# Kernel optimization log

Measured on AMD Instinct MI355X. Metric: run time of the kernel, lower is better.

## Reference

```python
import jax, jax.numpy as jnp
import numpy as np

B, T, H = 8, 8192, 512
E, R = 4, 16
SCALE = 0.04  # ~1/sqrt(H), keeps activations/logits in a sane range


def setup_inputs() -> dict:
    key = jax.random.key(0)
    ks = jax.random.split(key, 7)
    return {
        "x": jax.random.normal(ks[0], (B, T, H), jnp.float32),
        "gate_w": jax.random.normal(ks[1], (E, H), jnp.float32) * SCALE,
        "thr_w": jax.random.normal(ks[2], (1, H), jnp.float32) * SCALE,
        "fc1_w": jax.random.normal(ks[3], (E, H, H), jnp.float32) * SCALE,
        "lora_A": jax.random.normal(ks[4], (E, H, R), jnp.float32) * SCALE,
        "lora_B": jax.random.normal(ks[5], (E, R, H), jnp.float32) * SCALE,
        "fc2_w": jax.random.normal(ks[6], (E, H, H), jnp.float32) * SCALE,
    }


def reference(x, gate_w, thr_w, fc1_w, lora_A, lora_B, fc2_w):
    b, t, h = x.shape
    e = gate_w.shape[0]
    xf = x.reshape(-1, h)  # [N, H], N = B*T

    # Threshold-gated routing
    gate_logits = jax.nn.softmax(xf @ gate_w.T, axis=-1)          # [N, E]
    thresholds = jax.nn.sigmoid(xf @ thr_w.T) * (1.0 / e)         # [N, 1]
    adapted = gate_logits - thresholds                            # [N, E]
    selected = (adapted >= 0).astype(xf.dtype)                    # [N, E]
    weights = adapted * selected
    wsum = jnp.sum(weights, axis=-1, keepdims=True)
    wsum = jnp.where(wsum == 0, jnp.ones_like(wsum), wsum)
    weights = weights / wsum                                      # [N, E]

    # Experts: fc2(relu(fc1(x)) @ A @ B). Dense over all experts; the
    # weighted combine with zero weights matches the gather/scatter path.
    hidden = jax.nn.relu(jnp.einsum('ni,ehi->neh', xf, fc1_w))    # [N, E, H]
    lo = jnp.einsum('neh,ehr->ner', hidden, lora_A)               # [N, E, R]
    lo = jnp.einsum('ner,ero->neo', lo, lora_B)                   # [N, E, H]
    expert_out = jnp.einsum('neo,edo->ned', lo, fc2_w)            # [N, E, H]

    out = jnp.einsum('ne,ned->nd', weights, expert_out)           # [N, H]
    return out.reshape(b, t, h)
```

## Files before the change

kernel.cpp:

```cpp
#include <hip/hip_runtime.h>
#include <stdint.h>

#define NTOK 65536
#define HD   512
#define EXP  4
#define RK   16

typedef __attribute__((ext_vector_type(8)))  short short8;
typedef __attribute__((ext_vector_type(4)))  float f32x4;
typedef __attribute__((ext_vector_type(16))) float f32x16;

__device__ __forceinline__ unsigned short f2bf(float f) {
  union { float f; unsigned int u; } c; c.f = f;
  return (unsigned short)((c.u + 0x7fffu + ((c.u >> 16) & 1u)) >> 16);
}

__device__ __forceinline__ void gl_lds16(const void* g, void* l) {
  __builtin_amdgcn_global_load_lds((const __attribute__((address_space(1))) void*)g,
                                   (__attribute__((address_space(3))) void*)l, 16, 0, 0);
}

__global__ void convgate(const float* __restrict__ x, const float* __restrict__ gw,
                         const float* __restrict__ tw, unsigned short* __restrict__ xbo,
                         float* __restrict__ gates) {
  const int lane = threadIdx.x & 63;
  const int n = blockIdx.x * 4 + (threadIdx.x >> 6);
  const float4* xr = (const float4*)(x + (size_t)n * HD);
  const float4 xa = xr[lane * 2], xb = xr[lane * 2 + 1];
  ushort4 ua, ub;
  ua.x = f2bf(xa.x); ua.y = f2bf(xa.y); ua.z = f2bf(xa.z); ua.w = f2bf(xa.w);
  ub.x = f2bf(xb.x); ub.y = f2bf(xb.y); ub.z = f2bf(xb.z); ub.w = f2bf(xb.w);
  ushort4* xo = (ushort4*)(xbo + (size_t)n * HD);
  xo[lane * 2] = ua; xo[lane * 2 + 1] = ub;
  float s[5];
#pragma unroll
  for (int e = 0; e < 4; e++) {
    const float4* wr = (const float4*)(gw + e * HD);
    const float4 wa = wr[lane * 2], wb = wr[lane * 2 + 1];
    s[e] = xa.x * wa.x + xa.y * wa.y + xa.z * wa.z + xa.w * wa.w
         + xb.x * wb.x + xb.y * wb.y + xb.z * wb.z + xb.w * wb.w;
  }
  {
    const float4* wr = (const float4*)tw;
    const float4 wa = wr[lane * 2], wb = wr[lane * 2 + 1];
    s[4] = xa.x * wa.x + xa.y * wa.y + xa.z * wa.z + xa.w * wa.w
         + xb.x * wb.x + xb.y * wb.y + xb.z * wb.z + xb.w * wb.w;
  }
#pragma unroll
  for (int off = 32; off > 0; off >>= 1)
#pragma unroll
    for (int i = 0; i < 5; i++) s[i] += __shfl_xor(s[i], off, 64);
  float m = fmaxf(fmaxf(s[0], s[1]), fmaxf(s[2], s[3]));
  float e0 = expf(s[0] - m), e1 = expf(s[1] - m), e2 = expf(s[2] - m), e3 = expf(s[3] - m);
  float inv = 1.f / (e0 + e1 + e2 + e3);
  float thr = 0.25f / (1.f + expf(-s[4]));
  float a0 = e0 * inv - thr, a1 = e1 * inv - thr, a2 = e2 * inv - thr, a3 = e3 * inv - thr;
  float w0 = a0 > 0.f ? a0 : 0.f, w1 = a1 > 0.f ? a1 : 0.f;
  float w2 = a2 > 0.f ? a2 : 0.f, w3 = a3 > 0.f ? a3 : 0.f;
  float wsum = w0 + w1 + w2 + w3;
  wsum = (wsum == 0.f) ? 1.f : wsum;
  if (lane < 4) {
    float wv = lane == 0 ? w0 : lane == 1 ? w1 : lane == 2 ? w2 : w3;
    gates[(size_t)n * 4 + lane] = wv / wsum;
  }
}

__global__ void convk(const float* __restrict__ in, unsigned short* __restrict__ o, int n4) {
  int i = blockIdx.x * 256 + threadIdx.x;
  if (i < n4) {
    float4 v = ((const float4*)in)[i];
    ushort4 u;
    u.x = f2bf(v.x); u.y = f2bf(v.y); u.z = f2bf(v.z); u.w = f2bf(v.w);
    ((ushort4*)o)[i] = u;
  }
}

__global__ void prep_mt(const float* __restrict__ loraB, const float* __restrict__ fc2,
                        unsigned short* __restrict__ Mt) {
  int idx = blockIdx.x * 256 + threadIdx.x;
  int d  = idx & (HD - 1);
  int er = idx >> 9;
  int e = er >> 4, r = er & 15;
  const float4* B = (const float4*)(loraB + ((size_t)e * RK + r) * HD);
  const float4* F = (const float4*)(fc2 + ((size_t)e * HD + d) * HD);
  float a0 = 0.f, a1 = 0.f, a2 = 0.f, a3 = 0.f;
  for (int i = 0; i < HD / 4; i += 4) {
    float4 b0 = B[i],     f0 = F[i];
    float4 b1 = B[i + 1], f1 = F[i + 1];
    float4 b2 = B[i + 2], f2 = F[i + 2];
    float4 b3 = B[i + 3], f3 = F[i + 3];
    a0 += b0.x * f0.x + b0.y * f0.y + b0.z * f0.z + b0.w * f0.w;
    a1 += b1.x * f1.x + b1.y * f1.y + b1.z * f1.z + b1.w * f1.w;
    a2 += b2.x * f2.x + b2.y * f2.y + b2.z * f2.z + b2.w * f2.w;
    a3 += b3.x * f3.x + b3.y * f3.y + b3.z * f3.z + b3.w * f3.w;
  }
  Mt[d * 64 + er] = f2bf(a0 + a1 + a2 + a3);
}

__launch_bounds__(256, 4)
__global__ void fc1_lora(const unsigned short* __restrict__ xb,
                         const unsigned short* __restrict__ w1b,
                         const float* __restrict__ loraA,
                         float* __restrict__ lw) {
  __shared__ __align__(16) char smem[34816];
  const int bid = blockIdx.x;
  const int c = bid & 7, s = bid >> 3;
  const int eh = s & 15;
  const int e = eh >> 2, hq = eh & 3;
  const int ntile = ((s >> 4) << 3) | c;
  const int n0 = ntile * 128;
  const int tid = threadIdx.x;
  const int wave = tid >> 6, lane = tid & 63;
  const int l16 = lane & 15, quad = lane >> 4;
  const int l32 = lane & 31, half = lane >> 5;

  const unsigned short* xg = xb + (size_t)n0 * HD;
  const unsigned short* wg = w1b + ((size_t)e * HD + (size_t)hq * 128) * HD;

  char* ldsx = smem;
  char* ldsw = smem + 16384;

  const unsigned short* xsrc[4];
  const unsigned short* wsrc[4];
#pragma unroll
  for (int i = 0; i < 4; i++) {
    const int sl = tid + 256 * i;
    const int row = sl >> 3, g = (sl & 7) ^ (row & 7);
    xsrc[i] = xg + (size_t)row * HD + g * 8;
    wsrc[i] = wg + (size_t)row * HD + g * 8;
  }

  const int twave = (wave & 1) * 64;
  const int hwave = (wave >> 1) * 64;

  int axo[4][2], bxo[4][2];
#pragma unroll
  for (int kk = 0; kk < 4; kk++)
#pragma unroll
    for (int b = 0; b < 2; b++) {
      const int rowa = twave + b * 32 + l32;
      axo[kk][b] = (rowa * 8 + ((kk * 2 + half) ^ (rowa & 7))) * 16;
      const int rowb = hwave + b * 32 + l32;
      bxo[kk][b] = (rowb * 8 + ((kk * 2 + half) ^ (rowb & 7))) * 16;
    }

  f32x16 acc[2][2];
#pragma unroll
  for (int mb = 0; mb < 2; mb++)
#pragma unroll
    for (int nb = 0; nb < 2; nb++)
#pragma unroll
      for (int r = 0; r < 16; r++) acc[mb][nb][r] = 0.f;

  for (int ks = 0; ks < 8; ks++) {
    const int ko = ks * 64;
#pragma unroll
    for (int i = 0; i < 4; i++) {
      gl_lds16(xsrc[i] + ko, ldsx + (256 * i + wave * 64) * 16);
      gl_lds16(wsrc[i] + ko, ldsw + (256 * i + wave * 64) * 16);
    }
    __syncthreads();
#pragma unroll
    for (int kk = 0; kk < 4; kk++) {
      short8 af[2], bf[2];
#pragma unroll
      for (int mb = 0; mb < 2; mb++) af[mb] = *(const short8*)(ldsx + axo[kk][mb]);
#pragma unroll
      for (int nb = 0; nb < 2; nb++) bf[nb] = *(const short8*)(ldsw + bxo[kk][nb]);
#pragma unroll
      for (int mb = 0; mb < 2; mb++)
#pragma unroll
        for (int nb = 0; nb < 2; nb++)
          acc[mb][nb] = __builtin_amdgcn_mfma_f32_32x32x16_bf16(af[mb], bf[nb], acc[mb][nb], 0, 0, 0);
    }
    __syncthreads();
  }

  unsigned short* hsm = (unsigned short*)smem;
#pragma unroll
  for (int mb = 0; mb < 2; mb++)
#pragma unroll
    for (int nb = 0; nb < 2; nb++) {
      const int colh = hwave + nb * 32 + l32;
#pragma unroll
      for (int r = 0; r < 16; r++) {
        const int tok = twave + mb * 32 + 4 * half + (r & 3) + 8 * (r >> 2);
        float v = acc[mb][nb][r];
        v = v > 0.f ? v : 0.f;
        hsm[tok * 136 + colh] = f2bf(v);
      }
    }
  __syncthreads();

  const float* Ae = loraA + (size_t)e * HD * RK;
  const int hA0 = hq * 128;
  f32x4 lo[2];
#pragma unroll
  for (int mf = 0; mf < 2; mf++)
#pragma unroll
    for (int i = 0; i < 4; i++) lo[mf][i] = 0.f;
#pragma unroll
  for (int k2 = 0; k2 < 4; k2++) {
    short8 a2[2];
#pragma unroll
    for (int mf = 0; mf < 2; mf++) {
      const int tok = wave * 32 + mf * 16 + l16;
      a2[mf] = *(const short8*)(hsm + tok * 136 + k2 * 32 + quad * 8);
    }
    union { short8 v; unsigned short s[8]; } b2;
#pragma unroll
    for (int j = 0; j < 8; j++)
      b2.s[j] = f2bf(Ae[(size_t)(hA0 + k2 * 32 + quad * 8 + j) * RK + l16]);
#pragma unroll
    for (int mf = 0; mf < 2; mf++)
      lo[mf] = __builtin_amdgcn_mfma_f32_16x16x32_bf16(a2[mf], b2.v, lo[mf], 0, 0, 0);
  }
#pragma unroll
  for (int mf = 0; mf < 2; mf++)
#pragma unroll
    for (int i = 0; i < 4; i++)
      atomicAdd(lw + (size_t)(n0 + wave * 32 + mf * 16 + quad * 4 + i) * 64 + e * 16 + l16, lo[mf][i]);
}

__launch_bounds__(256, 2)
__global__ void combine_k(const float* __restrict__ lw, const float* __restrict__ gates,
                          const unsigned short* __restrict__ Mt, float* __restrict__ out) {
  __shared__ __align__(16) char smem[65536];
  const int n0 = blockIdx.x * 64;
  const int tid = threadIdx.x;
  const int wave = tid >> 6, lane = tid & 63, quad = lane >> 4, l16 = lane & 15;
#pragma unroll
  for (int i = 0; i < 16; i++) {
    const int slot = tid + 256 * i;
    const int row = slot >> 3;
    const int g = (slot & 7) ^ (row & 7);
    *(uint4*)(smem + slot * 16) = *(const uint4*)(Mt + row * 64 + g * 8);
  }
  __syncthreads();
  f32x4 acc[4][8];
#pragma unroll
  for (int a = 0; a < 4; a++)
#pragma unroll
    for (int b = 0; b < 8; b++)
#pragma unroll
      for (int i = 0; i < 4; i++) acc[a][b][i] = 0.f;
#pragma unroll
  for (int ks = 0; ks < 2; ks++) {
    short8 af[4], bfr[8];
#pragma unroll
    for (int mf = 0; mf < 4; mf++) {
      const int n = n0 + mf * 16 + l16;
      const float* lr = lw + (size_t)n * 64 + ks * 32 + quad * 8;
      float4 u0 = *(const float4*)lr;
      float4 u1 = *(const float4*)(lr + 4);
      const float g = gates[(size_t)n * 4 + ((ks * 32 + quad * 8) >> 4)];
      union { short8 v; unsigned short s[8]; } a;
      a.s[0] = f2bf(u0.x * g); a.s[1] = f2bf(u0.y * g);
      a.s[2] = f2bf(u0.z * g); a.s[3] = f2bf(u0.w * g);
      a.s[4] = f2bf(u1.x * g); a.s[5] = f2bf(u1.y * g);
      a.s[6] = f2bf(u1.z * g); a.s[7] = f2bf(u1.w * g);
      af[mf] = a.v;
    }
#pragma unroll
    for (int nf = 0; nf < 8; nf++) {
      const int row = wave * 128 + nf * 16 + l16;
      const int slot = row * 8 + ((ks * 4 + quad) ^ (row & 7));
      bfr[nf] = *(const short8*)(smem + slot * 16);
    }
#pragma unroll
    for (int mf = 0; mf < 4; mf++)
#pragma unroll
      for (int nf = 0; nf < 8; nf++)
        acc[mf][nf] = __builtin_amdgcn_mfma_f32_16x16x32_bf16(af[mf], bfr[nf], acc[mf][nf], 0, 0, 0);
  }
#pragma unroll
  for (int mf = 0; mf < 4; mf++)
#pragma unroll
    for (int nf = 0; nf < 8; nf++) {
      const int d = wave * 128 + nf * 16 + l16;
#pragma unroll
      for (int i = 0; i < 4; i++)
        out[(size_t)(n0 + mf * 16 + quad * 4 + i) * HD + d] = acc[mf][nf][i];
    }
}

extern "C" void kernel_launch(void* const* d_in, const int* in_sizes, int n_in,
                              void* d_out, int out_size, void* d_ws, size_t ws_size,
                              hipStream_t stream) {
  const float* x      = (const float*)d_in[0];
  const float* gate_w = (const float*)d_in[1];
  const float* thr_w  = (const float*)d_in[2];
  const float* fc1_w  = (const float*)d_in[3];
  const float* lora_A = (const float*)d_in[4];
  const float* lora_B = (const float*)d_in[5];
  const float* fc2_w  = (const float*)d_in[6];
  float* out = (float*)d_out;
  char* ws = (char*)d_ws;

  unsigned short* xbp = (unsigned short*)(ws);
  unsigned short* w1b = (unsigned short*)(ws + 67108864);
  unsigned short* Mt  = (unsigned short*)(ws + 69206016);
  float*          gts = (float*)(ws + 69271552);
  float*          lwp = (float*)(ws + 70320128);

  hipMemsetAsync(lwp, 0, (size_t)NTOK * 64 * sizeof(float), stream);
  convgate<<<NTOK / 4, 256, 0, stream>>>(x, gate_w, thr_w, xbp, gts);
  convk<<<1024, 256, 0, stream>>>(fc1_w, w1b, EXP * HD * HD / 4);
  prep_mt<<<128, 256, 0, stream>>>(lora_B, fc2_w, Mt);
  fc1_lora<<<8192, 256, 0, stream>>>(xbp, w1b, lora_A, lwp);
  combine_k<<<NTOK / 64, 256, 0, stream>>>(lwp, gts, Mt, out);
}
```

Measured before the change: 442.8 us.

## Enlarge fc1 tile to 256x256 with 4-stage async LDS pipeline

The fc1+LoRA-A kernel now uses 512-thread blocks computing 256 tokens by 256 hidden columns, with each wave owning a 128x64 sub-tile. The K loop is restructured into a four-buffer ring of 32-wide slices prefetched three steps ahead via global_load_lds, with explicit vmcnt waits, barriers and setprio around MFMA bursts. This is meant to hide global load latency and raise operand reuse per LDS byte. In exchange it uses about 132KB of LDS per block, so occupancy is lower and the hand-counted waitcnt schedule is fragile.

```diff
diff --git a/kernel.cpp b/kernel.cpp
--- a/kernel.cpp
+++ b/kernel.cpp
@@ -97,120 +97,144 @@
   Mt[d * 64 + er] = f2bf(a0 + a1 + a2 + a3);
 }
 
-__launch_bounds__(256, 4)
+__launch_bounds__(512, 2)
 __global__ void fc1_lora(const unsigned short* __restrict__ xb,
                          const unsigned short* __restrict__ w1b,
                          const float* __restrict__ loraA,
                          float* __restrict__ lw) {
-  __shared__ __align__(16) char smem[34816];
+  __shared__ __align__(16) char smem[135168];
   const int bid = blockIdx.x;
-  const int c = bid & 7, s = bid >> 3;
-  const int eh = s & 15;
-  const int e = eh >> 2, hq = eh & 3;
-  const int ntile = ((s >> 4) << 3) | c;
-  const int n0 = ntile * 128;
+  const int eh = bid & 7;
+  const int e = eh >> 1, hq = eh & 1;
+  const int ntile = bid >> 3;
+  const int n0 = ntile * 256;
   const int tid = threadIdx.x;
   const int wave = tid >> 6, lane = tid & 63;
   const int l16 = lane & 15, quad = lane >> 4;
   const int l32 = lane & 31, half = lane >> 5;
+  const int wr = wave >> 2, wc = wave & 3;
 
   const unsigned short* xg = xb + (size_t)n0 * HD;
-  const unsigned short* wg = w1b + ((size_t)e * HD + (size_t)hq * 128) * HD;
-
-  char* ldsx = smem;
-  char* ldsw = smem + 16384;
-
-  const unsigned short* xsrc[4];
-  const unsigned short* wsrc[4];
-#pragma unroll
-  for (int i = 0; i < 4; i++) {
-    const int sl = tid + 256 * i;
-    const int row = sl >> 3, g = (sl & 7) ^ (row & 7);
+  const unsigned short* wg = w1b + ((size_t)e * HD + (size_t)hq * 256) * HD;
+
+  const unsigned short* xsrc[2];
+  const unsigned short* wsrc[2];
+#pragma unroll
+  for (int i = 0; i < 2; i++) {
+    const int sl = tid + 512 * i;
+    const int row = sl >> 2, g = (sl & 3) ^ (row & 3);
     xsrc[i] = xg + (size_t)row * HD + g * 8;
     wsrc[i] = wg + (size_t)row * HD + g * 8;
   }
-
-  const int twave = (wave & 1) * 64;
-  const int hwave = (wave >> 1) * 64;
-
-  int axo[4][2], bxo[4][2];
-#pragma unroll
-  for (int kk = 0; kk < 4; kk++)
-#pragma unroll
-    for (int b = 0; b < 2; b++) {
-      const int rowa = twave + b * 32 + l32;
-      axo[kk][b] = (rowa * 8 + ((kk * 2 + half) ^ (rowa & 7))) * 16;
-      const int rowb = hwave + b * 32 + l32;
-      bxo[kk][b] = (rowb * 8 + ((kk * 2 + half) ^ (rowb & 7))) * 16;
-    }
-
-  f32x16 acc[2][2];
-#pragma unroll
-  for (int mb = 0; mb < 2; mb++)
+  const int wbase = wave * 1024;
+
+  int axo[2][4], bxo[2][2];
+#pragma unroll
+  for (int kk = 0; kk < 2; kk++) {
+#pragma unroll
+    for (int mb = 0; mb < 4; mb++) {
+      const int rowa = wr * 128 + mb * 32 + l32;
+      axo[kk][mb] = (rowa * 4 + ((kk * 2 + half) ^ (rowa & 3))) * 16;
+    }
+#pragma unroll
+    for (int nb = 0; nb < 2; nb++) {
+      const int rowb = wc * 64 + nb * 32 + l32;
+      bxo[kk][nb] = (rowb * 4 + ((kk * 2 + half) ^ (rowb & 3))) * 16;
+    }
+  }
+
+  f32x16 acc[4][2];
+#pragma unroll
+  for (int mb = 0; mb < 4; mb++)
 #pragma unroll
     for (int nb = 0; nb < 2; nb++)
 #pragma unroll
       for (int r = 0; r < 16; r++) acc[mb][nb][r] = 0.f;
 
-  for (int ks = 0; ks < 8; ks++) {
-    const int ko = ks * 64;
-#pragma unroll
-    for (int i = 0; i < 4; i++) {
-      gl_lds16(xsrc[i] + ko, ldsx + (256 * i + wave * 64) * 16);
-      gl_lds16(wsrc[i] + ko, ldsw + (256 * i + wave * 64) * 16);
-    }
-    __syncthreads();
-#pragma unroll
-    for (int kk = 0; kk < 4; kk++) {
-      short8 af[2], bf[2];
-#pragma unroll
-      for (int mb = 0; mb < 2; mb++) af[mb] = *(const short8*)(ldsx + axo[kk][mb]);
-#pragma unroll
-      for (int nb = 0; nb < 2; nb++) bf[nb] = *(const short8*)(ldsw + bxo[kk][nb]);
-#pragma unroll
-      for (int mb = 0; mb < 2; mb++)
+#pragma unroll
+  for (int tt = 0; tt < 3; tt++) {
+    char* As = smem + tt * 32768;
+#pragma unroll
+    for (int i = 0; i < 2; i++) gl_lds16(xsrc[i] + tt * 32, As + wbase + 8192 * i);
+#pragma unroll
+    for (int i = 0; i < 2; i++) gl_lds16(wsrc[i] + tt * 32, As + 16384 + wbase + 8192 * i);
+  }
+  asm volatile("s_waitcnt vmcnt(8)\n\ts_barrier" ::: "memory");
+  __builtin_amdgcn_sched_barrier(0);
+
+#pragma unroll
+  for (int t = 0; t < 16; t++) {
+    char* Ab = smem + (t & 3) * 32768;
+    char* Bb = Ab + 16384;
+    char* As = smem + ((t + 3) & 3) * 32768;
+    const int kos = (t + 3) * 32;
+#pragma unroll
+    for (int p = 0; p < 2; p++) {
+      short8 af[4], bf[2];
+#pragma unroll
+      for (int mb = 0; mb < 4; mb++) af[mb] = *(const short8*)(Ab + axo[p][mb]);
+#pragma unroll
+      for (int nb = 0; nb < 2; nb++) bf[nb] = *(const short8*)(Bb + bxo[p][nb]);
+      if (t < 13) {
+        gl_lds16(xsrc[p] + kos, As + wbase + 8192 * p);
+        gl_lds16(wsrc[p] + kos, As + 16384 + wbase + 8192 * p);
+      }
+      asm volatile("s_barrier" ::: "memory");
+      __builtin_amdgcn_s_setprio(1);
+#pragma unroll
+      for (int mb = 0; mb < 4; mb++)
 #pragma unroll
         for (int nb = 0; nb < 2; nb++)
           acc[mb][nb] = __builtin_amdgcn_mfma_f32_32x32x16_bf16(af[mb], bf[nb], acc[mb][nb], 0, 0, 0);
-    }
-    __syncthreads();
+      __builtin_amdgcn_s_setprio(0);
+    }
+    if (t < 13) {
+      asm volatile("s_waitcnt lgkmcnt(0)\n\ts_waitcnt vmcnt(8)\n\ts_barrier" ::: "memory");
+    } else if (t == 13) {
+      asm volatile("s_waitcnt lgkmcnt(0)\n\ts_waitcnt vmcnt(4)\n\ts_barrier" ::: "memory");
+    } else if (t == 14) {
+      asm volatile("s_waitcnt lgkmcnt(0)\n\ts_waitcnt vmcnt(0)\n\ts_barrier" ::: "memory");
+    } else {
+      asm volatile("s_waitcnt lgkmcnt(0)\n\ts_barrier" ::: "memory");
+    }
+    __builtin_amdgcn_sched_barrier(0);
   }
 
   unsigned short* hsm = (unsigned short*)smem;
 #pragma unroll
-  for (int mb = 0; mb < 2; mb++)
+  for (int mb = 0; mb < 4; mb++)
 #pragma unroll
     for (int nb = 0; nb < 2; nb++) {
-      const int colh = hwave + nb * 32 + l32;
+      const int colh = wc * 64 + nb * 32 + l32;
 #pragma unroll
       for (int r = 0; r < 16; r++) {
-        const int tok = twave + mb * 32 + 4 * half + (r & 3) + 8 * (r >> 2);
+        const int tok = wr * 128 + mb * 32 + 4 * half + (r & 3) + 8 * (r >> 2);
         float v = acc[mb][nb][r];
         v = v > 0.f ? v : 0.f;
-        hsm[tok * 136 + colh] = f2bf(v);
+        hsm[tok * 264 + colh] = f2bf(v);
       }
     }
   __syncthreads();
 
   const float* Ae = loraA + (size_t)e * HD * RK;
-  const int hA0 = hq * 128;
+  const int hA0 = hq * 256;
   f32x4 lo[2];
 #pragma unroll
   for (int mf = 0; mf < 2; mf++)
 #pragma unroll
     for (int i = 0; i < 4; i++) lo[mf][i] = 0.f;
 #pragma unroll
-  for (int k2 = 0; k2 < 4; k2++) {
+  for (int k2 = 0; k2 < 8; k2++) {
     short8 a2[2];
 #pragma unroll
     for (int mf = 0; mf < 2; mf++) {
       const int tok = wave * 32 + mf * 16 + l16;
-      a2[mf] = *(const short8*)(hsm + tok * 136 + k2 * 32 + quad * 8);
-    }
-    union { short8 v; unsigned short s[8]; } b2;
+      a2[mf] = *(const short8*)(hsm + tok * 264 + k2 * 32 + quad * 8);
+    }
+    union { short8 v; unsigned short sv[8]; } b2;
 #pragma unroll
     for (int j = 0; j < 8; j++)
-      b2.s[j] = f2bf(Ae[(size_t)(hA0 + k2 * 32 + quad * 8 + j) * RK + l16]);
+      b2.sv[j] = f2bf(Ae[(size_t)(hA0 + k2 * 32 + quad * 8 + j) * RK + l16]);
 #pragma unroll
     for (int mf = 0; mf < 2; mf++)
       lo[mf] = __builtin_amdgcn_mfma_f32_16x16x32_bf16(a2[mf], b2.v, lo[mf], 0, 0, 0);
@@ -307,6 +331,6 @@
   convgate<<<NTOK / 4, 256, 0, stream>>>(x, gate_w, thr_w, xbp, gts);
   convk<<<1024, 256, 0, stream>>>(fc1_w, w1b, EXP * HD * HD / 4);
   prep_mt<<<128, 256, 0, stream>>>(lora_B, fc2_w, Mt);
-  fc1_lora<<<8192, 256, 0, stream>>>(xbp, w1b, lora_A, lwp);
+  fc1_lora<<<2048, 512, 0, stream>>>(xbp, w1b, lora_A, lwp);
   combine_k<<<NTOK / 64, 256, 0, stream>>>(lwp, gts, Mt, out);
 }
```

After: 467.6 us. +5.6%, slower.
